# Performance work log

Hardware: AMD Instinct MI355X
Metric: run time of the kernel (lower is better)

The kernel has to match this reference:

```python
import jax, jax.numpy as jnp
import numpy as np

CHANNELS = 32
CONVOLUTIONS = 8
GIN_HIDDEN = 64
HIDDEN = 64
NODE_TYPES = 6
OUTPUT = 32
N_NODES = 200000
N_EDGES = 3200000
NUM_GRAPHS = 512
EPS = 1e-5


def setup_inputs() -> dict:
    key = jax.random.key(0)
    ks = jax.random.split(key, 16)
    x = jax.random.randint(ks[0], (N_NODES,), 0, NODE_TYPES)
    edge_index = jax.random.randint(ks[1], (2, N_EDGES), 0, N_NODES)
    batch = jnp.sort(jax.random.randint(ks[2], (N_NODES,), 0, NUM_GRAPHS))
    s = lambda fan_in: 1.0 / np.sqrt(fan_in)
    emb = jax.random.normal(ks[3], (NODE_TYPES, CHANNELS), jnp.float32)
    Wh = jax.random.uniform(ks[4], (CONVOLUTIONS, CHANNELS, GIN_HIDDEN), jnp.float32, -s(CHANNELS), s(CHANNELS))
    bh = jax.random.uniform(ks[5], (CONVOLUTIONS, GIN_HIDDEN), jnp.float32, -s(CHANNELS), s(CHANNELS))
    Wo = jax.random.uniform(ks[6], (CONVOLUTIONS, GIN_HIDDEN, CHANNELS), jnp.float32, -s(GIN_HIDDEN), s(GIN_HIDDEN))
    bo = jax.random.uniform(ks[7], (CONVOLUTIONS, CHANNELS), jnp.float32, -s(GIN_HIDDEN), s(GIN_HIDDEN))
    fin = (CONVOLUTIONS + 1) * CHANNELS
    W_hid = jax.random.uniform(ks[8], (fin, HIDDEN), jnp.float32, -s(fin), s(fin))
    b_hid = jax.random.uniform(ks[9], (HIDDEN,), jnp.float32, -s(fin), s(fin))
    W_out = jax.random.uniform(ks[10], (HIDDEN, OUTPUT), jnp.float32, -s(HIDDEN), s(HIDDEN))
    b_out = jax.random.uniform(ks[11], (OUTPUT,), jnp.float32, -s(HIDDEN), s(HIDDEN))
    return {"x": x, "edge_index": edge_index, "batch": batch, "emb": emb,
            "Wh": Wh, "bh": bh, "Wo": Wo, "bo": bo,
            "W_hid": W_hid, "b_hid": b_hid, "W_out": W_out, "b_out": b_out}


def reference(x, edge_index, batch, emb, Wh, bh, Wo, bo, W_hid, b_hid, W_out, b_out):
    n = x.shape[0]
    src, dst = edge_index[0], edge_index[1]
    counts = jax.ops.segment_sum(jnp.ones((n,), jnp.float32), batch,
                                 num_segments=NUM_GRAPHS)[:, None]  # [G,1]
    h = emb[x]  # [N, C]
    xs = [h]
    for i in range(CONVOLUTIONS):
        # GINConv (eps=0): MLP(x + sum_{j->i} x_j)
        aggr = jax.ops.segment_sum(h[src], dst, num_segments=n)
        z = h + aggr
        z = jax.nn.relu(z @ Wh[i] + bh[i]) @ Wo[i] + bo[i]
        # per-graph InstanceNorm (no affine, biased variance)
        mean = jax.ops.segment_sum(z, batch, num_segments=NUM_GRAPHS) / counts
        var = jax.ops.segment_sum(z * z, batch, num_segments=NUM_GRAPHS) / counts - mean * mean
        zn = (z - mean[batch]) * jax.lax.rsqrt(var[batch] + EPS)
        h = jax.nn.relu(h + zn)
        xs.append(h)
    feats = jnp.concatenate(xs, axis=1)  # [N, (CONVOLUTIONS+1)*C]
    pooled = jax.ops.segment_max(feats, batch, num_segments=NUM_GRAPHS)  # [G, 288]
    hid = jax.nn.relu(pooled @ W_hid + b_hid)
    return hid @ W_out + b_out  # [G, OUTPUT]
```

## Files before the change

kernel.cpp:

```cpp
#include <hip/hip_runtime.h>
#include <math.h>

#define NGRAPH 512
#define FEATS 288
#define EPS 1e-5f
#define NBAND 4

typedef __attribute__((ext_vector_type(8))) short short8v;
typedef __attribute__((ext_vector_type(8))) unsigned short ushort8v;
typedef __attribute__((ext_vector_type(4))) unsigned short ushort4v;
typedef __attribute__((ext_vector_type(4))) float float4v;

__device__ __forceinline__ unsigned short f2bf(float f) {
  unsigned int u = __float_as_uint(f);
  u += 0x7fff + ((u >> 16) & 1);
  return (unsigned short)(u >> 16);
}
__device__ __forceinline__ float bf2f(unsigned short u) {
  return __uint_as_float(((unsigned int)u) << 16);
}

__device__ __forceinline__ int srcband(int s, int bandsz) {
  return (s >= bandsz) + (s >= 2 * bandsz) + (s >= 3 * bandsz);
}

__device__ __forceinline__ void atomicMaxF(float* addr, float v) {
  if (v >= 0.f) atomicMax((int*)addr, __float_as_int(v));
  else atomicMin((unsigned int*)addr, __float_as_uint(v));
}

__global__ void k_init(float* __restrict__ pooled, float* __restrict__ counts,
                       float* __restrict__ stats, int* __restrict__ degseg,
                       int* __restrict__ typemask, unsigned int* __restrict__ curpk,
                       const float* __restrict__ Wh, const float* __restrict__ Wo,
                       unsigned short* __restrict__ whb, unsigned short* __restrict__ wob,
                       int N4, int N) {
  int i = blockIdx.x * blockDim.x + threadIdx.x;
  if (i < NGRAPH * FEATS) pooled[i] = -INFINITY;
  if (i < NGRAPH) { counts[i] = 0.f; typemask[i] = 0; }
  if (i < NGRAPH * 128) stats[i] = 0.f;
  if (i < N4) degseg[i] = 0;
  if (i < N) curpk[i] = 0u;

  if (blockIdx.x < 8) {
    int conv = blockIdx.x;
    const float* wh = Wh + (size_t)conv * 2048;
    const float* wo = Wo + (size_t)conv * 2048;
    unsigned short* oh = whb + (size_t)conv * 2048;
    unsigned short* oo = wob + (size_t)conv * 2048;
    for (int p = threadIdx.x; p < 2048; p += blockDim.x) {
      int rem = p & 511, l = rem >> 3, ii = rem & 7;
      int nt = p >> 9;
      int k = (l >> 4) * 8 + ii;
      int n = nt * 16 + (l & 15);
      oh[p] = f2bf(wh[k * 64 + n]);
      int blk = p >> 9, nt2 = blk >> 1, ks = blk & 1;
      int k2 = ks * 32 + (l >> 4) * 8 + ii;
      int n2 = nt2 * 16 + (l & 15);
      oo[p] = f2bf(wo[k2 * 32 + n2]);
    }
  }
}

__global__ __launch_bounds__(256) void k_embed(
    const int* __restrict__ x, const int* __restrict__ batch,
    const float* __restrict__ emb, unsigned short* __restrict__ hbf,
    int* __restrict__ typemask, float* __restrict__ counts, int N) {
  long t = (long)blockIdx.x * blockDim.x + threadIdx.x;
  int n = (int)(t >> 3), q = (int)(t & 7);
  int lane = threadIdx.x & 63;
  bool valid = (n < N);
  int g = 0, tt = 0;
  if (valid) {
    g = batch[n];
    tt = x[n];
    float4 e = *((const float4*)(emb + (size_t)tt * 32 + q * 4));
    ushort4v hb;
    hb[0] = f2bf(e.x); hb[1] = f2bf(e.y); hb[2] = f2bf(e.z); hb[3] = f2bf(e.w);
    *((ushort4v*)(hbf + (size_t)n * 32 + q * 4)) = hb;
  }
  int g0 = __shfl(g, 0);
  bool uniform = __all(valid) && __all(g == g0);
  int m = valid ? (1 << tt) : 0;
  if (uniform) {
    #pragma unroll
    for (int d = 1; d < 64; d <<= 1) m |= __shfl_xor(m, d);
    if (lane == 0) {
      atomicOr(&typemask[g0], m);
      atomicAdd(&counts[g0], 8.f);
    }
  } else if (valid && q == 0) {
    atomicOr(&typemask[g], m);
    atomicAdd(&counts[g], 1.f);
  }
}

__global__ void k_pool0(const int* __restrict__ typemask, const float* __restrict__ emb,
                        float* __restrict__ pooled) {
  int i = blockIdx.x * blockDim.x + threadIdx.x;
  if (i >= NGRAPH * 32) return;
  int g = i >> 5, c = i & 31;
  int m = typemask[g];
  float v = -INFINITY;
  #pragma unroll
  for (int t = 0; t < 6; t++)
    if (m & (1 << t)) v = fmaxf(v, emb[t * 32 + c]);
  pooled[(size_t)g * FEATS + c] = v;
}

__global__ void k_hist(const int* __restrict__ dst, const int* __restrict__ src,
                       int* __restrict__ degseg, int E, int eb,
                       int dband, int bandsz, int N) {
  int band = blockIdx.x / eb;
  int e = (blockIdx.x - band * eb) * blockDim.x + threadIdx.x;
  if (e >= E) return;
  int bandlo = band * dband;
  int bandhi = min(bandlo + dband, N);
  int d = dst[e];
  if (d < bandlo || d >= bandhi) return;
  int sb = srcband(src[e], bandsz);
  atomicAdd(&degseg[(size_t)d * 4 + sb], 1);
}

__global__ void k_scan_block(const int* __restrict__ deg, int* __restrict__ excl,
                             int* __restrict__ bsum, int N) {
  __shared__ int s[256];
  int i = blockIdx.x * 256 + threadIdx.x;
  int t = threadIdx.x;
  int v = (i < N) ? deg[i] : 0;
  s[t] = v;
  __syncthreads();
  for (int off = 1; off < 256; off <<= 1) {
    int add = (t >= off) ? s[t - off] : 0;
    __syncthreads();
    s[t] += add;
    __syncthreads();
  }
  if (i < N) excl[i] = s[t] - v;
  if (t == 255) bsum[blockIdx.x] = s[255];
}

__global__ void k_scan_bsum(int* __restrict__ bsum, int nb) {
  __shared__ int s[256];
  __shared__ int carry;
  int t = threadIdx.x;
  if (t == 0) carry = 0;
  __syncthreads();
  for (int base = 0; base < nb; base += 256) {
    int i = base + t;
    int v = (i < nb) ? bsum[i] : 0;
    s[t] = v;
    __syncthreads();
    for (int off = 1; off < 256; off <<= 1) {
      int add = (t >= off) ? s[t - off] : 0;
      __syncthreads();
      s[t] += add;
      __syncthreads();
    }
    if (i < nb) bsum[i] = s[t] - v + carry;
    __syncthreads();
    if (t == 0) carry += s[255];
    __syncthreads();
  }
}

__global__ void k_scan_add(int* __restrict__ excl, const int* __restrict__ bsum, int N) {
  int i = blockIdx.x * 256 + threadIdx.x;
  if (i < N) excl[i] = excl[i] + bsum[blockIdx.x];
}

__global__ void k_scatter(const int* __restrict__ src, const int* __restrict__ dst,
                          const int* __restrict__ rowseg, unsigned int* __restrict__ curpk,
                          unsigned short* __restrict__ adj, int E,
                          int eb, int dband, int bandsz, int N) {
  int band = blockIdx.x / eb;
  int e = (blockIdx.x - band * eb) * blockDim.x + threadIdx.x;
  if (e >= E) return;
  int bandlo = band * dband;
  int bandhi = min(bandlo + dband, N);
  int d = dst[e];
  if (d < bandlo || d >= bandhi) return;
  int s = src[e];
  int sb = srcband(s, bandsz);
  int seg = d * 4 + sb;
  unsigned int old = atomicAdd(&curpk[seg >> 2], 1u << ((seg & 3) * 8));
  int local = (int)((old >> ((seg & 3) * 8)) & 0xffu);
  int pos = rowseg[seg] + local;
  adj[pos] = (unsigned short)(s - sb * bandsz);
}

__global__ __launch_bounds__(256, 8) void k_conv(
    const unsigned short* __restrict__ hbf,
    const unsigned short* __restrict__ adj, const int* __restrict__ rowseg,
    const int* __restrict__ degseg,
    const unsigned short* __restrict__ whb, const float* __restrict__ bh,
    const unsigned short* __restrict__ wob, const float* __restrict__ bo,
    const int* __restrict__ batch, unsigned short* __restrict__ z2,
    float* __restrict__ stats, float* __restrict__ statsOther,
    int bandsz, int N) {
  __shared__ unsigned short sWhB[4 * 64 * 8];
  __shared__ unsigned short sWoB[2 * 2 * 64 * 8];
  __shared__ unsigned short st[4][16][72];

  {
    int zi = blockIdx.x * 256 + threadIdx.x;
    if (zi < NGRAPH * 64) statsOther[zi] = 0.f;
    int p = threadIdx.x * 8;
    *((ushort8v*)&sWhB[p]) = *((const ushort8v*)&whb[p]);
    *((ushort8v*)&sWoB[p]) = *((const ushort8v*)&wob[p]);
  }
  __syncthreads();

  int wid = threadIdx.x >> 6;
  int lane = threadIdx.x & 63;
  int col = lane & 15;
  int grp = lane >> 4;
  int gwave = blockIdx.x * 4 + wid;
  int wstride = gridDim.x * 4;
  int ntiles = (N + 15) >> 4;

  const unsigned short* __restrict__ qb = hbf + grp * 8;

  float keepT[2][8];
  #pragma unroll
  for (int t = 0; t < 2; t++)
    #pragma unroll
    for (int i = 0; i < 8; i++) keepT[t][i] = 0.f;

  #pragma unroll
  for (int b = 0; b < 4; b++) {
    const unsigned short* __restrict__ bq = qb + (size_t)(b * bandsz) * 32;
    #pragma unroll
    for (int t = 0; t < 2; t++) {
      int tile = gwave + t * wstride;
      if (tile >= ntiles) continue;
      int node = tile * 16 + col;
      int s0 = 0, dg = 0;
      if (node < N) {
        s0 = rowseg[(size_t)node * 4 + b];
        dg = degseg[(size_t)node * 4 + b];
      }
      int k = 0;
      for (; k + 4 <= dg; k += 4) {
        int sA = adj[s0 + k + 0];
        int sB = adj[s0 + k + 1];
        int sC = adj[s0 + k + 2];
        int sD = adj[s0 + k + 3];
        ushort8v a = *((const ushort8v*)(bq + (size_t)sA * 32));
        ushort8v bv = *((const ushort8v*)(bq + (size_t)sB * 32));
        ushort8v c = *((const ushort8v*)(bq + (size_t)sC * 32));
        ushort8v d = *((const ushort8v*)(bq + (size_t)sD * 32));
        #pragma unroll
        for (int i = 0; i < 8; i++) {
          keepT[t][i] += bf2f(a[i]);
          keepT[t][i] += bf2f(bv[i]);
          keepT[t][i] += bf2f(c[i]);
          keepT[t][i] += bf2f(d[i]);
        }
      }
      if (k + 2 <= dg) {
        int sA = adj[s0 + k + 0];
        int sB = adj[s0 + k + 1];
        ushort8v a = *((const ushort8v*)(bq + (size_t)sA * 32));
        ushort8v bv = *((const ushort8v*)(bq + (size_t)sB * 32));
        #pragma unroll
        for (int i = 0; i < 8; i++) {
          keepT[t][i] += bf2f(a[i]);
          keepT[t][i] += bf2f(bv[i]);
        }
        k += 2;
      }
      if (k < dg) {
        int sA = adj[s0 + k];
        ushort8v a = *((const ushort8v*)(bq + (size_t)sA * 32));
        #pragma unroll
        for (int i = 0; i < 8; i++) keepT[t][i] += bf2f(a[i]);
      }
    }
  }

  #pragma unroll
  for (int t = 0; t < 2; t++) {
    int tile = gwave + t * wstride;
    if (tile >= ntiles) continue;
    int base = tile * 16;
    int node = base + col;

    float zf[8];
    if (node < N) {
      ushort8v own = *((const ushort8v*)(hbf + (size_t)node * 32 + grp * 8));
      #pragma unroll
      for (int i = 0; i < 8; i++) zf[i] = bf2f(own[i]) + keepT[t][i];
    } else {
      #pragma unroll
      for (int i = 0; i < 8; i++) zf[i] = 0.f;
    }
    short8v afrag;
    #pragma unroll
    for (int i = 0; i < 8; i++) afrag[i] = (short)f2bf(zf[i]);

    #pragma unroll
    for (int nt = 0; nt < 4; nt++) {
      float b = bh[nt * 16 + col];
      float4v acc1 = {b, b, b, b};
      short8v bfrag = *((const short8v*)&sWhB[(nt * 64 + lane) * 8]);
      acc1 = __builtin_amdgcn_mfma_f32_16x16x32_bf16(afrag, bfrag, acc1, 0, 0, 0);
      #pragma unroll
      for (int r = 0; r < 4; r++) {
        st[wid][grp * 4 + r][nt * 16 + col] = f2bf(fmaxf(acc1[r], 0.f));
      }
    }

    short8v a2[2];
    #pragma unroll
    for (int ks = 0; ks < 2; ks++)
      a2[ks] = *((const short8v*)&st[wid][col][ks * 32 + grp * 8]);

    float4v acc2[2];
    #pragma unroll
    for (int nt2 = 0; nt2 < 2; nt2++) {
      float b = bo[nt2 * 16 + col];
      acc2[nt2] = (float4v){b, b, b, b};
      #pragma unroll
      for (int ks = 0; ks < 2; ks++) {
        short8v bfrag = *((const short8v*)&sWoB[((nt2 * 2 + ks) * 64 + lane) * 8]);
        acc2[nt2] = __builtin_amdgcn_mfma_f32_16x16x32_bf16(a2[ks], bfrag, acc2[nt2], 0, 0, 0);
      }
    }

    #pragma unroll
    for (int nt2 = 0; nt2 < 2; nt2++) {
      #pragma unroll
      for (int r = 0; r < 4; r++) {
        int nd = base + grp * 4 + r;
        if (nd < N)
          __builtin_nontemporal_store(f2bf(acc2[nt2][r]), z2 + (size_t)nd * 32 + nt2 * 16 + col);
      }
    }

    int g0 = batch[base];
    int gLast = batch[min(base + 15, N - 1)];
    if ((base + 16 <= N) && g0 == gLast) {
      #pragma unroll
      for (int nt2 = 0; nt2 < 2; nt2++) {
        float s = acc2[nt2][0] + acc2[nt2][1] + acc2[nt2][2] + acc2[nt2][3];
        float ss = acc2[nt2][0] * acc2[nt2][0] + acc2[nt2][1] * acc2[nt2][1]
                 + acc2[nt2][2] * acc2[nt2][2] + acc2[nt2][3] * acc2[nt2][3];
        s += __shfl_xor(s, 16); s += __shfl_xor(s, 32);
        ss += __shfl_xor(ss, 16); ss += __shfl_xor(ss, 32);
        if (grp == 0) {
          atomicAdd(&stats[(size_t)g0 * 64 + nt2 * 16 + col], s);
          atomicAdd(&stats[(size_t)g0 * 64 + 32 + nt2 * 16 + col], ss);
        }
      }
    } else {
      #pragma unroll
      for (int nt2 = 0; nt2 < 2; nt2++) {
        #pragma unroll
        for (int r = 0; r < 4; r++) {
          int nd = base + grp * 4 + r;
          if (nd < N) {
            int g = batch[nd];
            float v = acc2[nt2][r];
            atomicAdd(&stats[(size_t)g * 64 + nt2 * 16 + col], v);
            atomicAdd(&stats[(size_t)g * 64 + 32 + nt2 * 16 + col], v * v);
          }
        }
      }
    }
  }
}

__global__ __launch_bounds__(256, 4) void k_conv0(
    const unsigned short* __restrict__ hbf,
    const unsigned short* __restrict__ adj, const int* __restrict__ rowseg,
    const int* __restrict__ degseg,
    const int* __restrict__ x, const float* __restrict__ emb,
    const unsigned short* __restrict__ whb, const float* __restrict__ bh,
    const unsigned short* __restrict__ wob, const float* __restrict__ bo,
    const int* __restrict__ batch, unsigned short* __restrict__ z2,
    float* __restrict__ stats, float* __restrict__ statsOther,
    int bandsz, int N) {
  __shared__ unsigned short sWhB[4 * 64 * 8];
  __shared__ unsigned short sWoB[2 * 2 * 64 * 8];
  __shared__ unsigned short st[4][16][72];
  __shared__ float sEmb[6][32];

  {
    int zi = blockIdx.x * 256 + threadIdx.x;
    if (zi < NGRAPH * 64) statsOther[zi] = 0.f;
    int p = threadIdx.x * 8;
    *((ushort8v*)&sWhB[p]) = *((const ushort8v*)&whb[p]);
    *((ushort8v*)&sWoB[p]) = *((const ushort8v*)&wob[p]);
    if (threadIdx.x < 192) ((float*)sEmb)[threadIdx.x] = emb[threadIdx.x];
  }
  __syncthreads();

  int wid = threadIdx.x >> 6;
  int lane = threadIdx.x & 63;
  int tile = blockIdx.x * 4 + wid;
  int base = tile * 16;
  if (base >= N) return;
  int col = lane & 15;
  int grp = lane >> 4;
  int node = base + col;

  int sArr[4] = {0, 0, 0, 0}, dArr[4] = {0, 0, 0, 0};
  if (node < N) {
    int4 s4 = *((const int4*)(rowseg + (size_t)node * 4));
    int4 d4 = *((const int4*)(degseg + (size_t)node * 4));
    sArr[0] = s4.x; sArr[1] = s4.y; sArr[2] = s4.z; sArr[3] = s4.w;
    dArr[0] = d4.x; dArr[1] = d4.y; dArr[2] = d4.z; dArr[3] = d4.w;
  }

  float c0 = 0.f, c1 = 0.f, c2 = 0.f, c3 = 0.f, c4 = 0.f, c5 = 0.f;
  #pragma unroll
  for (int b = 0; b < 4; b++) {
    int s0 = sArr[b], dg = dArr[b];
    int bbase = b * bandsz;
    for (int j = grp; j < dg; j += 4) {
      int sA = bbase + (int)adj[s0 + j];
      int tA = x[sA];
      c0 += (tA == 0) ? 1.f : 0.f; c1 += (tA == 1) ? 1.f : 0.f;
      c2 += (tA == 2) ? 1.f : 0.f; c3 += (tA == 3) ? 1.f : 0.f;
      c4 += (tA == 4) ? 1.f : 0.f; c5 += (tA == 5) ? 1.f : 0.f;
    }
  }

  c0 += __shfl_xor(c0, 16); c0 += __shfl_xor(c0, 32);
  c1 += __shfl_xor(c1, 16); c1 += __shfl_xor(c1, 32);
  c2 += __shfl_xor(c2, 16); c2 += __shfl_xor(c2, 32);
  c3 += __shfl_xor(c3, 16); c3 += __shfl_xor(c3, 32);
  c4 += __shfl_xor(c4, 16); c4 += __shfl_xor(c4, 32);
  c5 += __shfl_xor(c5, 16); c5 += __shfl_xor(c5, 32);

  float zf[8];
  if (node < N) {
    ushort8v own = *((const ushort8v*)(hbf + (size_t)node * 32 + grp * 8));
    #pragma unroll
    for (int i = 0; i < 8; i++) {
      int ch = grp * 8 + i;
      float v = bf2f(own[i]);
      v = fmaf(c0, sEmb[0][ch], v);
      v = fmaf(c1, sEmb[1][ch], v);
      v = fmaf(c2, sEmb[2][ch], v);
      v = fmaf(c3, sEmb[3][ch], v);
      v = fmaf(c4, sEmb[4][ch], v);
      v = fmaf(c5, sEmb[5][ch], v);
      zf[i] = v;
    }
  } else {
    #pragma unroll
    for (int i = 0; i < 8; i++) zf[i] = 0.f;
  }
  short8v afrag;
  #pragma unroll
  for (int i = 0; i < 8; i++) afrag[i] = (short)f2bf(zf[i]);

  #pragma unroll
  for (int nt = 0; nt < 4; nt++) {
    float b = bh[nt * 16 + col];
    float4v acc1 = {b, b, b, b};
    short8v bfrag = *((const short8v*)&sWhB[(nt * 64 + lane) * 8]);
    acc1 = __builtin_amdgcn_mfma_f32_16x16x32_bf16(afrag, bfrag, acc1, 0, 0, 0);
    #pragma unroll
    for (int r = 0; r < 4; r++) {
      st[wid][grp * 4 + r][nt * 16 + col] = f2bf(fmaxf(acc1[r], 0.f));
    }
  }

  short8v a2[2];
  #pragma unroll
  for (int ks = 0; ks < 2; ks++)
    a2[ks] = *((const short8v*)&st[wid][col][ks * 32 + grp * 8]);

  float4v acc2[2];
  #pragma unroll
  for (int nt2 = 0; nt2 < 2; nt2++) {
    float b = bo[nt2 * 16 + col];
    acc2[nt2] = (float4v){b, b, b, b};
    #pragma unroll
    for (int ks = 0; ks < 2; ks++) {
      short8v bfrag = *((const short8v*)&sWoB[((nt2 * 2 + ks) * 64 + lane) * 8]);
      acc2[nt2] = __builtin_amdgcn_mfma_f32_16x16x32_bf16(a2[ks], bfrag, acc2[nt2], 0, 0, 0);
    }
  }

  #pragma unroll
  for (int nt2 = 0; nt2 < 2; nt2++) {
    #pragma unroll
    for (int r = 0; r < 4; r++) {
      int nd = base + grp * 4 + r;
      if (nd < N)
        __builtin_nontemporal_store(f2bf(acc2[nt2][r]), z2 + (size_t)nd * 32 + nt2 * 16 + col);
    }
  }

  int g0 = batch[base];
  int gLast = batch[min(base + 15, N - 1)];
  if ((base + 16 <= N) && g0 == gLast) {
    #pragma unroll
    for (int nt2 = 0; nt2 < 2; nt2++) {
      float s = acc2[nt2][0] + acc2[nt2][1] + acc2[nt2][2] + acc2[nt2][3];
      float ss = acc2[nt2][0] * acc2[nt2][0] + acc2[nt2][1] * acc2[nt2][1]
               + acc2[nt2][2] * acc2[nt2][2] + acc2[nt2][3] * acc2[nt2][3];
      s += __shfl_xor(s, 16); s += __shfl_xor(s, 32);
      ss += __shfl_xor(ss, 16); ss += __shfl_xor(ss, 32);
      if (grp == 0) {
        atomicAdd(&stats[(size_t)g0 * 64 + nt2 * 16 + col], s);
        atomicAdd(&stats[(size_t)g0 * 64 + 32 + nt2 * 16 + col], ss);
      }
    }
  } else {
    #pragma unroll
    for (int nt2 = 0; nt2 < 2; nt2++) {
      #pragma unroll
      for (int r = 0; r < 4; r++) {
        int nd = base + grp * 4 + r;
        if (nd < N) {
          int g = batch[nd];
          float v = acc2[nt2][r];
          atomicAdd(&stats[(size_t)g * 64 + nt2 * 16 + col], v);
          atomicAdd(&stats[(size_t)g * 64 + 32 + nt2 * 16 + col], v * v);
        }
      }
    }
  }
}

__global__ __launch_bounds__(256) void k_norm(
    unsigned short* __restrict__ hbf, const unsigned short* __restrict__ z2,
    const float* __restrict__ stats, const float* __restrict__ counts,
    const int* __restrict__ batch, float* __restrict__ pooled, int conv, int N) {
  long t = (long)blockIdx.x * blockDim.x + threadIdx.x;
  int n = (int)(t >> 3), q = (int)(t & 7);
  int lane = threadIdx.x & 63;
  bool valid = (n < N);

  int g = 0;
  float r0 = -INFINITY, r1 = -INFINITY, r2 = -INFINITY, r3 = -INFINITY;
  if (valid) {
    g = batch[n];
    float cnt = counts[g];
    float4 sv = *((const float4*)(stats + (size_t)g * 64 + q * 4));
    float4 qv = *((const float4*)(stats + (size_t)g * 64 + 32 + q * 4));
    float m0 = 0.f, m1 = 0.f, m2 = 0.f, m3 = 0.f;
    float i0 = 0.f, i1 = 0.f, i2 = 0.f, i3 = 0.f;
    if (cnt > 0.f) {
      m0 = sv.x / cnt; m1 = sv.y / cnt; m2 = sv.z / cnt; m3 = sv.w / cnt;
      i0 = rsqrtf(fmaxf(qv.x / cnt - m0 * m0, 0.f) + EPS);
      i1 = rsqrtf(fmaxf(qv.y / cnt - m1 * m1, 0.f) + EPS);
      i2 = rsqrtf(fmaxf(qv.z / cnt - m2 * m2, 0.f) + EPS);
      i3 = rsqrtf(fmaxf(qv.w / cnt - m3 * m3, 0.f) + EPS);
    }
    ushort4v hb = *((const ushort4v*)(hbf + (size_t)n * 32 + q * 4));
    ushort4v zv = *((const ushort4v*)(z2 + (size_t)n * 32 + q * 4));
    r0 = fmaxf(bf2f(hb[0]) + (bf2f(zv[0]) - m0) * i0, 0.f);
    r1 = fmaxf(bf2f(hb[1]) + (bf2f(zv[1]) - m1) * i1, 0.f);
    r2 = fmaxf(bf2f(hb[2]) + (bf2f(zv[2]) - m2) * i2, 0.f);
    r3 = fmaxf(bf2f(hb[3]) + (bf2f(zv[3]) - m3) * i3, 0.f);
    hb[0] = f2bf(r0); hb[1] = f2bf(r1); hb[2] = f2bf(r2); hb[3] = f2bf(r3);
    *((ushort4v*)(hbf + (size_t)n * 32 + q * 4)) = hb;
  }

  int g0 = __shfl(g, 0);
  bool uniform = __all(valid) && __all(g == g0);
  if (uniform) {
    float m0 = r0, m1 = r1, m2 = r2, m3 = r3;
    #pragma unroll
    for (int d = 8; d < 64; d <<= 1) {
      m0 = fmaxf(m0, __shfl_xor(m0, d));
      m1 = fmaxf(m1, __shfl_xor(m1, d));
      m2 = fmaxf(m2, __shfl_xor(m2, d));
      m3 = fmaxf(m3, __shfl_xor(m3, d));
    }
    if (lane < 8) {
      float* poolrow = pooled + (size_t)g0 * FEATS + (conv + 1) * 32 + lane * 4;
      atomicMaxF(poolrow + 0, m0);
      atomicMaxF(poolrow + 1, m1);
      atomicMaxF(poolrow + 2, m2);
      atomicMaxF(poolrow + 3, m3);
    }
  } else if (valid) {
    float* poolrow = pooled + (size_t)g * FEATS + (conv + 1) * 32 + q * 4;
    atomicMaxF(poolrow + 0, r0);
    atomicMaxF(poolrow + 1, r1);
    atomicMaxF(poolrow + 2, r2);
    atomicMaxF(poolrow + 3, r3);
  }
}

__global__ __launch_bounds__(64) void k_head(
    const float* __restrict__ pooled, const float* __restrict__ W_hid,
    const float* __restrict__ b_hid, const float* __restrict__ W_out,
    const float* __restrict__ b_out, float* __restrict__ out) {
  __shared__ float sp[FEATS];
  __shared__ float sh[64];
  int g = blockIdx.x;
  for (int i = threadIdx.x; i < FEATS; i += 64) sp[i] = pooled[(size_t)g * FEATS + i];
  __syncthreads();
  int j = threadIdx.x;
  float acc = b_hid[j];
  for (int k = 0; k < FEATS; k++) acc = fmaf(sp[k], W_hid[k * 64 + j], acc);
  sh[j] = fmaxf(acc, 0.f);
  __syncthreads();
  if (j < 32) {
    float o = b_out[j];
    #pragma unroll
    for (int k = 0; k < 64; k++) o = fmaf(sh[k], W_out[k * 32 + j], o);
    out[(size_t)g * 32 + j] = o;
  }
}

extern "C" void kernel_launch(void* const* d_in, const int* in_sizes, int n_in,
                              void* d_out, int out_size, void* d_ws, size_t ws_size,
                              hipStream_t stream) {
  const int* x      = (const int*)d_in[0];
  const int* edge   = (const int*)d_in[1];
  const int* batch  = (const int*)d_in[2];
  const float* emb  = (const float*)d_in[3];
  const float* Wh   = (const float*)d_in[4];
  const float* bh   = (const float*)d_in[5];
  const float* Wo   = (const float*)d_in[6];
  const float* bo   = (const float*)d_in[7];
  const float* W_hid = (const float*)d_in[8];
  const float* b_hid = (const float*)d_in[9];
  const float* W_out = (const float*)d_in[10];
  const float* b_out = (const float*)d_in[11];
  float* out = (float*)d_out;

  int N = in_sizes[0];
  int E = in_sizes[1] / 2;
  const int* src = edge;
  const int* dst = edge + E;

  int N4 = N * 4;
  int bandsz = (N + NBAND - 1) / NBAND;

  float* ws = (float*)d_ws;
  size_t off = 0;
  unsigned short* z2 = (unsigned short*)(ws + off); off += (size_t)N * 16;
  float* pooled  = ws + off; off += (size_t)NGRAPH * FEATS;
  float* stats   = ws + off; off += (size_t)NGRAPH * 128;
  float* counts  = ws + off; off += NGRAPH;
  unsigned short* hbf = (unsigned short*)(ws + off); off += (size_t)N * 16;
  unsigned short* whb = (unsigned short*)(ws + off); off += 8192;
  unsigned short* wob = (unsigned short*)(ws + off); off += 8192;
  int* iws = (int*)(ws + off);
  size_t ioff = 0;
  int* degseg   = iws + ioff; ioff += N4;
  int* rowseg   = iws + ioff; ioff += N4;
  unsigned int* curpk = (unsigned int*)(iws + ioff); ioff += N;
  unsigned short* adj = (unsigned short*)(iws + ioff); ioff += (E + 1) / 2;
  int* bsum     = iws + ioff; ioff += 4096;
  int* typemask = iws + ioff; ioff += NGRAPH;

  int eb = (E + 255) / 256;
  int nb4 = (N4 + 255) / 256;
  int nb8 = (int)(((size_t)N * 8 + 255) / 256);
  int tiles = (N + 15) / 16;
  int mb = (tiles + 3) / 4;
  int ib = nb4;
  if (ib < (NGRAPH * FEATS + 255) / 256) ib = (NGRAPH * FEATS + 255) / 256;

  int dband = (N + NBAND - 1) / NBAND;

  k_init<<<ib, 256, 0, stream>>>(pooled, counts, stats, degseg, typemask, curpk,
                                 Wh, Wo, whb, wob, N4, N);
  k_embed<<<nb8, 256, 0, stream>>>(x, batch, emb, hbf, typemask, counts, N);
  k_pool0<<<(NGRAPH * 32 + 255) / 256, 256, 0, stream>>>(typemask, emb, pooled);

  k_hist<<<NBAND * eb, 256, 0, stream>>>(dst, src, degseg, E, eb, dband, bandsz, N);
  k_scan_block<<<nb4, 256, 0, stream>>>(degseg, rowseg, bsum, N4);
  k_scan_bsum<<<1, 256, 0, stream>>>(bsum, nb4);
  k_scan_add<<<nb4, 256, 0, stream>>>(rowseg, bsum, N4);
  k_scatter<<<NBAND * eb, 256, 0, stream>>>(src, dst, rowseg, curpk, adj, E, eb, dband, bandsz, N);

  const int GCONV = 2048;

  for (int i = 0; i < 8; i++) {
    float* sCur = stats + (size_t)(i & 1) * NGRAPH * 64;
    float* sOth = stats + (size_t)((i + 1) & 1) * NGRAPH * 64;
    if (i == 0) {
      k_conv0<<<mb, 256, 0, stream>>>(hbf, adj, rowseg, degseg, x, emb,
                                      whb, bh, wob, bo,
                                      batch, z2, sCur, sOth, bandsz, N);
    } else {
      k_conv<<<GCONV, 256, 0, stream>>>(hbf, adj, rowseg, degseg,
                                        whb + (size_t)i * 2048, bh + (size_t)i * 64,
                                        wob + (size_t)i * 2048, bo + (size_t)i * 32,
                                        batch, z2, sCur, sOth, bandsz, N);
    }
    k_norm<<<nb8, 256, 0, stream>>>(hbf, z2, sCur, counts, batch, pooled, i, N);
  }
  k_head<<<NGRAPH, 64, 0, stream>>>(pooled, W_hid, b_hid, W_out, b_out, out);
}
```

Baseline: 955.0 us.

## Build CSR via dst-bucket binning with LDS histogram and LDS-staged scatter

Replaces the banded global-atomic histogram and scatter passes over all edges with a binning pass. Edges are first sorted into coarse destination buckets in a packed buffer. Per-sub-range blocks then compute degrees with shared-memory atomics and assemble each adjacency slice in LDS before writing it out contiguously. This is meant to avoid the repeated full-edge reads per band and the scattered global atomics and writes. The new path adds an intermediate edge buffer with fixed capacity, and each bucket is re-read by 8 sub-range blocks. The old path is kept as a fallback when workspace or size limits are not met.

```diff
diff --git a/kernel.cpp b/kernel.cpp
--- a/kernel.cpp
+++ b/kernel.cpp
@@ -5,6 +5,11 @@
 #define FEATS 288
 #define EPS 1e-5f
 #define NBAND 4
+#define MAXBUCK 32
+#define BREP 4
+#define BSHIFT 13
+#define SUBR 1024
+#define IMGCAP 20480
 
 typedef __attribute__((ext_vector_type(8))) short short8v;
 typedef __attribute__((ext_vector_type(8))) unsigned short ushort8v;
@@ -32,6 +37,7 @@
 __global__ void k_init(float* __restrict__ pooled, float* __restrict__ counts,
                        float* __restrict__ stats, int* __restrict__ degseg,
                        int* __restrict__ typemask, unsigned int* __restrict__ curpk,
+                       int* __restrict__ bucketcnt,
                        const float* __restrict__ Wh, const float* __restrict__ Wo,
                        unsigned short* __restrict__ whb, unsigned short* __restrict__ wob,
                        int N4, int N) {
@@ -41,6 +47,7 @@
   if (i < NGRAPH * 128) stats[i] = 0.f;
   if (i < N4) degseg[i] = 0;
   if (i < N) curpk[i] = 0u;
+  if (i < BREP * MAXBUCK) bucketcnt[i] = 0;
 
   if (blockIdx.x < 8) {
     int conv = blockIdx.x;
@@ -108,6 +115,131 @@
   pooled[(size_t)g * FEATS + c] = v;
 }
 
+__global__ __launch_bounds__(256) void k_bin(
+    const int* __restrict__ src, const int* __restrict__ dst, int E,
+    int cap4, int* __restrict__ bucketcnt, unsigned int* __restrict__ ebuf,
+    int bandsz) {
+  __shared__ int lcnt[MAXBUCK];
+  __shared__ int gbase[MAXBUCK];
+  for (int i = threadIdx.x; i < MAXBUCK; i += 256) lcnt[i] = 0;
+  __syncthreads();
+  int e0 = blockIdx.x * 2048 + threadIdx.x;
+  int bArr[8], rArr[8];
+  unsigned int pArr[8];
+  #pragma unroll
+  for (int it = 0; it < 8; it++) {
+    int e = e0 + it * 256;
+    bArr[it] = -1;
+    if (e < E) {
+      int d = dst[e];
+      int s = src[e];
+      int b = d >> BSHIFT;
+      int sb = srcband(s, bandsz);
+      pArr[it] = ((unsigned int)(d & ((1 << BSHIFT) - 1)) << 18)
+               | ((unsigned int)sb << 16) | (unsigned int)(s - sb * bandsz);
+      rArr[it] = atomicAdd(&lcnt[b], 1);
+      bArr[it] = b;
+    }
+  }
+  __syncthreads();
+  int rep = blockIdx.x & (BREP - 1);
+  if (threadIdx.x < MAXBUCK) {
+    int b = threadIdx.x;
+    int c = lcnt[b];
+    gbase[b] = (c > 0) ? atomicAdd(&bucketcnt[rep * MAXBUCK + b], c) : 0;
+  }
+  __syncthreads();
+  #pragma unroll
+  for (int it = 0; it < 8; it++) {
+    if (bArr[it] >= 0) {
+      int b = bArr[it];
+      int pos = gbase[b] + rArr[it];
+      if (pos < cap4)
+        ebuf[((size_t)b * BREP + rep) * cap4 + pos] = pArr[it];
+    }
+  }
+}
+
+__global__ __launch_bounds__(1024) void k_histL(
+    const unsigned int* __restrict__ ebuf, const int* __restrict__ bucketcnt,
+    int cap4, int* __restrict__ degseg, int N) {
+  __shared__ unsigned int cpk[SUBR];
+  int p = blockIdx.x >> 3;
+  int j = blockIdx.x & 7;
+  int node0 = (p << BSHIFT) + j * SUBR;
+  if (node0 >= N) return;
+  int nEnd = min(node0 + SUBR, N);
+  for (int i = threadIdx.x; i < SUBR; i += 1024) cpk[i] = 0u;
+  __syncthreads();
+  for (int rep = 0; rep < BREP; rep++) {
+    int c = min(bucketcnt[rep * MAXBUCK + p], cap4);
+    const unsigned int* base = ebuf + ((size_t)p * BREP + rep) * cap4;
+    for (int idx = threadIdx.x; idx < c; idx += 1024) {
+      unsigned int pk = base[idx];
+      int node = (p << BSHIFT) + (int)(pk >> 18);
+      if (node >= node0 && node < nEnd) {
+        int sb = (int)((pk >> 16) & 3u);
+        atomicAdd(&cpk[node - node0], 1u << (sb * 8));
+      }
+    }
+  }
+  __syncthreads();
+  for (int i = threadIdx.x; i < nEnd - node0; i += 1024) {
+    unsigned int v = cpk[i];
+    int* dp = degseg + (size_t)(node0 + i) * 4;
+    dp[0] = (int)(v & 0xffu);
+    dp[1] = (int)((v >> 8) & 0xffu);
+    dp[2] = (int)((v >> 16) & 0xffu);
+    dp[3] = (int)(v >> 24);
+  }
+}
+
+__global__ __launch_bounds__(1024) void k_scatL(
+    const unsigned int* __restrict__ ebuf, const int* __restrict__ bucketcnt,
+    int cap4, const int* __restrict__ rowseg, unsigned int* __restrict__ curpk,
+    unsigned short* __restrict__ adj, int E, int N) {
+  __shared__ unsigned short img[IMGCAP];
+  __shared__ unsigned int cpk[SUBR];
+  int p = blockIdx.x >> 3;
+  int j = blockIdx.x & 7;
+  int node0 = (p << BSHIFT) + j * SUBR;
+  if (node0 >= N) return;
+  int nEnd = min(node0 + SUBR, N);
+  int imgbase = rowseg[(size_t)node0 * 4];
+  int imgend = (nEnd < N) ? rowseg[(size_t)nEnd * 4] : E;
+  int isz = imgend - imgbase;
+  bool lds = (isz <= IMGCAP);
+  for (int i = threadIdx.x; i < SUBR; i += 1024) cpk[i] = 0u;
+  __syncthreads();
+  for (int rep = 0; rep < BREP; rep++) {
+    int c = min(bucketcnt[rep * MAXBUCK + p], cap4);
+    const unsigned int* base = ebuf + ((size_t)p * BREP + rep) * cap4;
+    for (int idx = threadIdx.x; idx < c; idx += 1024) {
+      unsigned int pk = base[idx];
+      int node = (p << BSHIFT) + (int)(pk >> 18);
+      if (node >= node0 && node < nEnd) {
+        int sb = (int)((pk >> 16) & 3u);
+        int seg = node * 4 + sb;
+        unsigned short srel = (unsigned short)(pk & 0xffffu);
+        if (lds) {
+          unsigned int old = atomicAdd(&cpk[node - node0], 1u << (sb * 8));
+          int rank = (int)((old >> (sb * 8)) & 0xffu);
+          img[rowseg[seg] + rank - imgbase] = srel;
+        } else {
+          unsigned int old = atomicAdd(&curpk[seg >> 2], 1u << ((seg & 3) * 8));
+          int rank = (int)((old >> ((seg & 3) * 8)) & 0xffu);
+          adj[rowseg[seg] + rank] = srel;
+        }
+      }
+    }
+  }
+  __syncthreads();
+  if (lds) {
+    for (int i = threadIdx.x; i < isz; i += 1024)
+      adj[imgbase + i] = img[i];
+  }
+}
+
 __global__ void k_hist(const int* __restrict__ dst, const int* __restrict__ src,
                        int* __restrict__ degseg, int E, int eb,
                        int dband, int bandsz, int N) {
@@ -120,53 +252,6 @@
   if (d < bandlo || d >= bandhi) return;
   int sb = srcband(src[e], bandsz);
   atomicAdd(&degseg[(size_t)d * 4 + sb], 1);
-}
-
-__global__ void k_scan_block(const int* __restrict__ deg, int* __restrict__ excl,
-                             int* __restrict__ bsum, int N) {
-  __shared__ int s[256];
-  int i = blockIdx.x * 256 + threadIdx.x;
-  int t = threadIdx.x;
-  int v = (i < N) ? deg[i] : 0;
-  s[t] = v;
-  __syncthreads();
-  for (int off = 1; off < 256; off <<= 1) {
-    int add = (t >= off) ? s[t - off] : 0;
-    __syncthreads();
-    s[t] += add;
-    __syncthreads();
-  }
-  if (i < N) excl[i] = s[t] - v;
-  if (t == 255) bsum[blockIdx.x] = s[255];
-}
-
-__global__ void k_scan_bsum(int* __restrict__ bsum, int nb) {
-  __shared__ int s[256];
-  __shared__ int carry;
-  int t = threadIdx.x;
-  if (t == 0) carry = 0;
-  __syncthreads();
-  for (int base = 0; base < nb; base += 256) {
-    int i = base + t;
-    int v = (i < nb) ? bsum[i] : 0;
-    s[t] = v;
-    __syncthreads();
-    for (int off = 1; off < 256; off <<= 1) {
-      int add = (t >= off) ? s[t - off] : 0;
-      __syncthreads();
-      s[t] += add;
-      __syncthreads();
-    }
-    if (i < nb) bsum[i] = s[t] - v + carry;
-    __syncthreads();
-    if (t == 0) carry += s[255];
-    __syncthreads();
-  }
-}
-
-__global__ void k_scan_add(int* __restrict__ excl, const int* __restrict__ bsum, int N) {
-  int i = blockIdx.x * 256 + threadIdx.x;
-  if (i < N) excl[i] = excl[i] + bsum[blockIdx.x];
 }
 
 __global__ void k_scatter(const int* __restrict__ src, const int* __restrict__ dst,
@@ -185,8 +270,54 @@
   int seg = d * 4 + sb;
   unsigned int old = atomicAdd(&curpk[seg >> 2], 1u << ((seg & 3) * 8));
   int local = (int)((old >> ((seg & 3) * 8)) & 0xffu);
-  int pos = rowseg[seg] + local;
-  adj[pos] = (unsigned short)(s - sb * bandsz);
+  adj[rowseg[seg] + local] = (unsigned short)(s - sb * bandsz);
+}
+
+__global__ void k_scan_block(const int* __restrict__ deg, int* __restrict__ excl,
+                             int* __restrict__ bsum, int N) {
+  __shared__ int s[256];
+  int i = blockIdx.x * 256 + threadIdx.x;
+  int t = threadIdx.x;
+  int v = (i < N) ? deg[i] : 0;
+  s[t] = v;
+  __syncthreads();
+  for (int off = 1; off < 256; off <<= 1) {
+    int add = (t >= off) ? s[t - off] : 0;
+    __syncthreads();
+    s[t] += add;
+    __syncthreads();
+  }
+  if (i < N) excl[i] = s[t] - v;
+  if (t == 255) bsum[blockIdx.x] = s[255];
+}
+
+__global__ void k_scan_bsum(int* __restrict__ bsum, int nb) {
+  __shared__ int s[256];
+  __shared__ int carry;
+  int t = threadIdx.x;
+  if (t == 0) carry = 0;
+  __syncthreads();
+  for (int base = 0; base < nb; base += 256) {
+    int i = base + t;
+    int v = (i < nb) ? bsum[i] : 0;
+    s[t] = v;
+    __syncthreads();
+    for (int off = 1; off < 256; off <<= 1) {
+      int add = (t >= off) ? s[t - off] : 0;
+      __syncthreads();
+      s[t] += add;
+      __syncthreads();
+    }
+    if (i < nb) bsum[i] = s[t] - v + carry;
+    __syncthreads();
+    if (t == 0) carry += s[255];
+    __syncthreads();
+  }
+}
+
+__global__ void k_scan_add(int* __restrict__ excl, const int* __restrict__ bsum, int N) {
+  int i = blockIdx.x * 256 + threadIdx.x;
+  if (i < N) excl[i] = excl[i] + bsum[blockIdx.x];
 }
 
 __global__ __launch_bounds__(256, 8) void k_conv(
@@ -636,6 +767,8 @@
 
   int N4 = N * 4;
   int bandsz = (N + NBAND - 1) / NBAND;
+  int nbuck = (N + (1 << BSHIFT) - 1) >> BSHIFT;
+  int cap4 = E / (nbuck * BREP) + 8000;
 
   float* ws = (float*)d_ws;
   size_t off = 0;
@@ -654,8 +787,13 @@
   unsigned short* adj = (unsigned short*)(iws + ioff); ioff += (E + 1) / 2;
   int* bsum     = iws + ioff; ioff += 4096;
   int* typemask = iws + ioff; ioff += NGRAPH;
+  int* bucketcnt = iws + ioff; ioff += BREP * MAXBUCK;
+  unsigned int* ebuf = (unsigned int*)(iws + ioff); ioff += (size_t)nbuck * BREP * cap4;
+  bool fastCSR = ((off + ioff) * sizeof(float) <= ws_size) && (nbuck <= MAXBUCK)
+               && (bandsz < 65536);
 
   int eb = (E + 255) / 256;
+  int eb8 = (E + 2047) / 2048;
   int nb4 = (N4 + 255) / 256;
   int nb8 = (int)(((size_t)N * 8 + 255) / 256);
   int tiles = (N + 15) / 16;
@@ -666,15 +804,26 @@
   int dband = (N + NBAND - 1) / NBAND;
 
   k_init<<<ib, 256, 0, stream>>>(pooled, counts, stats, degseg, typemask, curpk,
-                                 Wh, Wo, whb, wob, N4, N);
+                                 bucketcnt, Wh, Wo, whb, wob, N4, N);
   k_embed<<<nb8, 256, 0, stream>>>(x, batch, emb, hbf, typemask, counts, N);
   k_pool0<<<(NGRAPH * 32 + 255) / 256, 256, 0, stream>>>(typemask, emb, pooled);
 
-  k_hist<<<NBAND * eb, 256, 0, stream>>>(dst, src, degseg, E, eb, dband, bandsz, N);
-  k_scan_block<<<nb4, 256, 0, stream>>>(degseg, rowseg, bsum, N4);
-  k_scan_bsum<<<1, 256, 0, stream>>>(bsum, nb4);
-  k_scan_add<<<nb4, 256, 0, stream>>>(rowseg, bsum, N4);
-  k_scatter<<<NBAND * eb, 256, 0, stream>>>(src, dst, rowseg, curpk, adj, E, eb, dband, bandsz, N);
+  if (fastCSR) {
+    k_bin<<<eb8, 256, 0, stream>>>(src, dst, E, cap4, bucketcnt, ebuf, bandsz);
+    k_histL<<<nbuck * 8, 1024, 0, stream>>>(ebuf, bucketcnt, cap4, degseg, N);
+    k_scan_block<<<nb4, 256, 0, stream>>>(degseg, rowseg, bsum, N4);
+    k_scan_bsum<<<1, 256, 0, stream>>>(bsum, nb4);
+    k_scan_add<<<nb4, 256, 0, stream>>>(rowseg, bsum, N4);
+    k_scatL<<<nbuck * 8, 1024, 0, stream>>>(ebuf, bucketcnt, cap4, rowseg, curpk,
+                                            adj, E, N);
+  } else {
+    k_hist<<<NBAND * eb, 256, 0, stream>>>(dst, src, degseg, E, eb, dband, bandsz, N);
+    k_scan_block<<<nb4, 256, 0, stream>>>(degseg, rowseg, bsum, N4);
+    k_scan_bsum<<<1, 256, 0, stream>>>(bsum, nb4);
+    k_scan_add<<<nb4, 256, 0, stream>>>(rowseg, bsum, N4);
+    k_scatter<<<NBAND * eb, 256, 0, stream>>>(src, dst, rowseg, curpk, adj, E, eb,
+                                              dband, bandsz, N);
+  }
 
   const int GCONV = 2048;
 
```

Measured after the change: 841.1 us. -11.9%, faster.
